# Performance work log

Measured on AMD Instinct MI355X. Metric: run time of the kernel, lower is better.

Reference implementation:

```python
import jax, jax.numpy as jnp
import numpy as np

VOCAB, D, SLOTS, K = 50257, 512, 16, 3
B, T_FULL = 64, 2049
EPS_LN = 1e-5


def setup_inputs() -> dict:
    key = jax.random.key(0)
    ks = jax.random.split(key, 12)
    u = jax.random.uniform(ks[0], (B, T_FULL - 1), jnp.float32)
    gumbel = -jnp.log(-jnp.log(u + 1e-8) + 1e-8)
    s = 0.02
    return {
        "seq": jax.random.randint(ks[1], (B, T_FULL), 0, VOCAB),
        "temperature": jnp.ones((), jnp.float32),
        "gumbel": gumbel,
        "embed": jax.random.normal(ks[2], (VOCAB, D), jnp.float32) * s,
        "W1": jax.random.normal(ks[3], (D, 2 * D), jnp.float32) * s,
        "b1": jnp.zeros((2 * D,), jnp.float32),
        "W2": jax.random.normal(ks[4], (2 * D, D), jnp.float32) * s,
        "b2": jnp.zeros((D,), jnp.float32),
        "gamma": jnp.ones((D,), jnp.float32),
        "beta": jnp.zeros((D,), jnp.float32),
        "Wg": jax.random.normal(ks[5], (D,), jnp.float32) * s,
        "bg": jnp.zeros((), jnp.float32),
        "Wr": jax.random.normal(ks[6], (D, D), jnp.float32) * s,
        "br": jnp.zeros((D,), jnp.float32),
        "Wo": jax.random.normal(ks[7], (D, VOCAB), jnp.float32) * s,
        "bo": jnp.zeros((VOCAB,), jnp.float32),
    }


def reference(seq, temperature, gumbel, embed, W1, b1, W2, b2, gamma, beta, Wg, bg, Wr, br, Wo, bo):
    # Encoder: embed -> FFN residual -> LayerNorm
    h = embed[seq]                                        # [B, T+1, D]
    ff = jnp.maximum(h @ W1 + b1, 0.0) @ W2 + b2
    x = h + ff
    mu = jnp.mean(x, -1, keepdims=True)
    var = jnp.mean((x - mu) ** 2, -1, keepdims=True)
    hiddens = (x - mu) * jax.lax.rsqrt(var + EPS_LN) * gamma + beta

    context = hiddens[:, :-1, :]                          # [B, T, D]
    gate = context @ Wg + bg                              # [B, T]

    # gumbel top-k with straight-through mask (forward value = hard mask)
    perturbed = (gate + gumbel) / temperature
    _, idx = jax.lax.top_k(perturbed, K)                  # [B, K]
    mask = jnp.zeros_like(gate).at[jnp.arange(B)[:, None], idx].set(1.0)
    soft = jax.nn.softmax(perturbed, axis=-1)
    sel = mask + soft - jax.lax.stop_gradient(soft)

    # gather selected hidden states, scatter_add into memory slots
    gw = jnp.take_along_axis(sel, idx, axis=1)            # [B, K]
    gh = jnp.take_along_axis(context, idx[..., None], axis=1)  # [B, K, D]
    weighted = gh * gw[..., None]
    slot_idx = jnp.arange(K) % SLOTS
    mem = jnp.zeros((B, SLOTS, D), hiddens.dtype).at[:, slot_idx, :].add(weighted)

    # attention read with last-position query
    q = hiddens[:, -1, :] @ Wr + br                       # [B, D]
    scores = jnp.einsum('bsd,bd->bs', mem, q)
    attn = jax.nn.softmax(scores, axis=-1)
    ctx = jnp.einsum('bs,bsd->bd', attn, mem)
    return ctx @ Wo + bo                                  # [B, vocab]
```

## Files before the change

kernel.cpp:

```cpp
#include <hip/hip_runtime.h>
#include <math.h>

#define TFULL 2049
#define TCTX  2048
#define Vm    50257

typedef __attribute__((ext_vector_type(8))) short bf16x8;
typedef __attribute__((ext_vector_type(4))) float f32x4;

__device__ __forceinline__ float wred64(float v){
  #pragma unroll
  for (int m = 1; m < 64; m <<= 1) v += __shfl_xor(v, m, 64);
  return v;
}
__device__ __forceinline__ short bf16_rn(float x){
  union { float f; unsigned u; } c; c.f = x;
  unsigned r = c.u + 0x7fff + ((c.u >> 16) & 1);
  return (short)(r >> 16);
}
__device__ __forceinline__ float bf16_f(short s){
  union { float f; unsigned u; } c; c.u = ((unsigned)(unsigned short)s) << 16;
  return c.f;
}

#define FMA4(ACC_, S_, W_)                         \
  (ACC_).x = fmaf((S_), (W_).x, (ACC_).x);         \
  (ACC_).y = fmaf((S_), (W_).y, (ACC_).y);         \
  (ACC_).z = fmaf((S_), (W_).z, (ACC_).z);         \
  (ACC_).w = fmaf((S_), (W_).w, (ACC_).w);

__global__ void k0_setup(const float* __restrict__ gamma, const float* __restrict__ beta,
                         const float* __restrict__ Wg, float* __restrict__ scal){
  const int t = threadIdx.x;
  float wg = Wg[t];
  float g  = gamma[t]*wg, bw = beta[t]*wg;
  scal[2 + t] = g;
  g = wred64(g); bw = wred64(bw);
  __shared__ float ra[8], rb[8];
  if ((t & 63) == 0){ ra[t>>6] = g; rb[t>>6] = bw; }
  __syncthreads();
  if (t == 0){
    float G = 0.f, Bw = 0.f;
    #pragma unroll
    for (int i = 0; i < 8; ++i){ G += ra[i]; Bw += rb[i]; }
    scal[0] = G; scal[1] = Bw;
  }
}

__global__ __launch_bounds__(256) void kpack(const float* __restrict__ W, int N, int KB,
                                             short* __restrict__ hi, short* __restrict__ lo){
  int i = blockIdx.x*256 + threadIdx.x;
  if (i >= KB*N*4) return;
  int kq = i & 3;
  int n  = (i >> 2) % N;
  int kb = i / (N*4);
  const float* src = W + (kb*32 + kq*8)*N + n;
  bf16x8 h8, l8;
  #pragma unroll
  for (int j = 0; j < 8; ++j){
    float w = src[j*N];
    short h = bf16_rn(w);
    h8[j] = h;
    l8[j] = bf16_rn(w - bf16_f(h));
  }
  *(bf16x8*)(hi + i*8) = h8;
  *(bf16x8*)(lo + i*8) = l8;
}

__global__ __launch_bounds__(512, 2) void k1_main(
    const int*   __restrict__ seq,   const float* __restrict__ temp,
    const float* __restrict__ gumbel,const float* __restrict__ embed,
    const short* __restrict__ W1h,   const short* __restrict__ W1l,
    const float* __restrict__ b1,
    const short* __restrict__ W2h,   const short* __restrict__ W2l,
    const float* __restrict__ b2,
    const float* __restrict__ gamma, const float* __restrict__ beta,
    const float* __restrict__ bg,
    const float* __restrict__ scal,
    float* __restrict__ pert, float* __restrict__ qh)
{
  __shared__ short Ah[8*2560];
  __shared__ short Al[8*2560];
  __shared__ short Rbuf[32768];
  __shared__ float Xq[512];
  __shared__ int   srow[64];
  __shared__ float redS1[512], redS2[512], redSG[512];
  __shared__ float redMu[64], redRs[64];

  short* Rh = Rbuf;
  short* Rl = Rbuf + 16384;

  const int t    = threadIdx.x;
  const int tile = blockIdx.x;
  const int lane = t & 63;
  const int wv   = t >> 6;
  const int mrow = lane & 15;
  const int kq   = lane >> 4;
  const int crow0 = kq*4;

  if (t < 64) srow[t] = seq[tile*64 + t];
  __syncthreads();

  const f32x4* __restrict__ embv = (const f32x4*)embed;

  auto stageA = [&](int hh){
    #pragma unroll
    for (int k = 0; k < 8; ++k){
      int idx = k*512 + t;
      int tok = idx >> 6, c4 = idx & 63;
      f32x4 v = __builtin_nontemporal_load(embv + srow[tok]*128 + hh*64 + c4);
      int dl = c4*4;
      int base = (dl>>5)*2560 + tok*40 + ((dl>>3)&3)*8 + (dl&7);
      short h0 = bf16_rn(v[0]), h1 = bf16_rn(v[1]), h2 = bf16_rn(v[2]), h3 = bf16_rn(v[3]);
      Ah[base+0] = h0; Ah[base+1] = h1; Ah[base+2] = h2; Ah[base+3] = h3;
      Al[base+0] = bf16_rn(v[0] - bf16_f(h0));
      Al[base+1] = bf16_rn(v[1] - bf16_f(h1));
      Al[base+2] = bf16_rn(v[2] - bf16_f(h2));
      Al[base+3] = bf16_rn(v[3] - bf16_f(h3));
    }
  };

  f32x4 ff[4][4];
  #pragma unroll
  for (int i = 0; i < 4; ++i)
    #pragma unroll
    for (int j = 0; j < 4; ++j) ff[i][j] = (f32x4){0.f,0.f,0.f,0.f};

  for (int ch = 0; ch < 4; ++ch){
    f32x4 acc[2][4];
    #pragma unroll
    for (int i = 0; i < 2; ++i)
      #pragma unroll
      for (int j = 0; j < 4; ++j) acc[i][j] = (f32x4){0.f,0.f,0.f,0.f};

    auto g1 = [&](int hh){
      #pragma unroll 4
      for (int kbr = 0; kbr < 8; ++kbr){
        bf16x8 ah[4], al[4];
        #pragma unroll
        for (int mt = 0; mt < 4; ++mt){
          ah[mt] = *(const bf16x8*)(Ah + kbr*2560 + (mrow + 16*mt)*40 + kq*8);
          al[mt] = *(const bf16x8*)(Al + kbr*2560 + (mrow + 16*mt)*40 + kq*8);
        }
        int kbg = hh*8 + kbr;
        #pragma unroll
        for (int nt = 0; nt < 2; ++nt){
          int n = ch*256 + wv*32 + nt*16 + mrow;
          int off = ((kbg*1024 + n)*4 + kq)*8;
          bf16x8 bh = *(const bf16x8*)(W1h + off);
          bf16x8 bl = *(const bf16x8*)(W1l + off);
          #pragma unroll
          for (int mt = 0; mt < 4; ++mt){
            acc[nt][mt] = __builtin_amdgcn_mfma_f32_16x16x32_bf16(ah[mt], bh, acc[nt][mt], 0,0,0);
            acc[nt][mt] = __builtin_amdgcn_mfma_f32_16x16x32_bf16(al[mt], bh, acc[nt][mt], 0,0,0);
            acc[nt][mt] = __builtin_amdgcn_mfma_f32_16x16x32_bf16(ah[mt], bl, acc[nt][mt], 0,0,0);
          }
        }
      }
    };

    stageA(0);
    __syncthreads();
    g1(0);
    __syncthreads();
    stageA(1);
    __syncthreads();
    g1(1);
    __syncthreads();

    #pragma unroll
    for (int nt = 0; nt < 2; ++nt){
      int jcol = wv*32 + nt*16 + mrow;
      float bb = b1[ch*256 + jcol];
      int rbase = (jcol>>5)*2048 + ((jcol>>3)&3)*8 + (jcol&7);
      #pragma unroll
      for (int mt = 0; mt < 4; ++mt){
        #pragma unroll
        for (int r = 0; r < 4; ++r){
          int tok = mt*16 + crow0 + r;
          float a = fmaxf(acc[nt][mt][r] + bb, 0.f);
          short h = bf16_rn(a);
          Rh[rbase + tok*32] = h;
          Rl[rbase + tok*32] = bf16_rn(a - bf16_f(h));
        }
      }
    }
    __syncthreads();

    #pragma unroll 2
    for (int kb = 0; kb < 8; ++kb){
      bf16x8 rh[4], rl[4];
      #pragma unroll
      for (int mt = 0; mt < 4; ++mt){
        rh[mt] = *(const bf16x8*)(Rh + kb*2048 + (mrow + 16*mt)*32 + kq*8);
        rl[mt] = *(const bf16x8*)(Rl + kb*2048 + (mrow + 16*mt)*32 + kq*8);
      }
      int kbg = ch*8 + kb;
      #pragma unroll
      for (int nt = 0; nt < 4; ++nt){
        int n = wv*64 + nt*16 + mrow;
        int off = ((kbg*512 + n)*4 + kq)*8;
        bf16x8 bh = *(const bf16x8*)(W2h + off);
        bf16x8 bl = *(const bf16x8*)(W2l + off);
        #pragma unroll
        for (int mt = 0; mt < 4; ++mt){
          ff[nt][mt] = __builtin_amdgcn_mfma_f32_16x16x32_bf16(rh[mt], bh, ff[nt][mt], 0,0,0);
          ff[nt][mt] = __builtin_amdgcn_mfma_f32_16x16x32_bf16(rl[mt], bh, ff[nt][mt], 0,0,0);
          ff[nt][mt] = __builtin_amdgcn_mfma_f32_16x16x32_bf16(rh[mt], bl, ff[nt][mt], 0,0,0);
        }
      }
    }
  }

  __syncthreads();
  float* hbuf = (float*)Rbuf;
  #pragma unroll
  for (int k = 0; k < 8; ++k){
    int idx = k*512 + t;
    int tok = idx >> 6, c4 = idx & 63;
    f32x4 v = __builtin_nontemporal_load(embv + srow[tok]*128 + c4);
    f32x4 hv;
    #pragma unroll
    for (int j = 0; j < 4; ++j){
      short hi = bf16_rn(v[j]);
      hv[j] = bf16_f(hi) + bf16_f(bf16_rn(v[j] - bf16_f(hi)));
    }
    *(f32x4*)(hbuf + tok*256 + c4*4) = hv;
  }
  __syncthreads();

  const float G1 = scal[0], BW = scal[1];
  const float* gWg = scal + 2;
  const float bgv  = bg[0];
  const float invT = 1.0f / temp[0];
  int rem  = (tile*64) % 2049;
  int qtok = 2048 - rem;

  float ps1[4][4], ps2[4][4], psg[4][4];
  #pragma unroll
  for (int mt = 0; mt < 4; ++mt)
    #pragma unroll
    for (int r = 0; r < 4; ++r){ ps1[mt][r]=0.f; ps2[mt][r]=0.f; psg[mt][r]=0.f; }

  #pragma unroll
  for (int nt = 0; nt < 4; ++nt){
    int d = wv*64 + nt*16 + mrow;
    float b2v = b2[d];
    float gw  = gWg[d];
    if (wv >= 4){
      int abase = ((d - 256)>>5)*2560 + ((d>>3)&3)*8 + (d&7);
      #pragma unroll
      for (int mt = 0; mt < 4; ++mt){
        #pragma unroll
        for (int r = 0; r < 4; ++r){
          int tok = mt*16 + crow0 + r;
          float h = bf16_f(Ah[abase + tok*40]) + bf16_f(Al[abase + tok*40]);
          float x = h + ff[nt][mt][r] + b2v;
          ps1[mt][r] += x;
          ps2[mt][r] = fmaf(x, x, ps2[mt][r]);
          psg[mt][r] = fmaf(x, gw, psg[mt][r]);
          if (tok == qtok) Xq[d] = x;
        }
      }
    } else {
      #pragma unroll
      for (int mt = 0; mt < 4; ++mt){
        #pragma unroll
        for (int r = 0; r < 4; ++r){
          int tok = mt*16 + crow0 + r;
          float h = hbuf[tok*256 + d];
          float x = h + ff[nt][mt][r] + b2v;
          ps1[mt][r] += x;
          ps2[mt][r] = fmaf(x, x, ps2[mt][r]);
          psg[mt][r] = fmaf(x, gw, psg[mt][r]);
          if (tok == qtok) Xq[d] = x;
        }
      }
    }
  }
  #pragma unroll
  for (int mt = 0; mt < 4; ++mt){
    #pragma unroll
    for (int r = 0; r < 4; ++r){
      float a = ps1[mt][r], b = ps2[mt][r], c = psg[mt][r];
      #pragma unroll
      for (int m = 1; m < 16; m <<= 1){
        a += __shfl_xor(a, m, 64);
        b += __shfl_xor(b, m, 64);
        c += __shfl_xor(c, m, 64);
      }
      if (mrow == 0){
        int tok = mt*16 + crow0 + r;
        redS1[tok*8 + wv] = a;
        redS2[tok*8 + wv] = b;
        redSG[tok*8 + wv] = c;
      }
    }
  }
  __syncthreads();

  if (t < 64){
    float S1 = 0.f, S2 = 0.f, SG = 0.f;
    #pragma unroll
    for (int w = 0; w < 8; ++w){
      S1 += redS1[t*8 + w];
      S2 += redS2[t*8 + w];
      SG += redSG[t*8 + w];
    }
    float mu  = S1 * (1.f/512.f);
    float var = S2 * (1.f/512.f) - mu*mu;
    float rs  = rsqrtf(var + 1e-5f);
    redMu[t] = mu; redRs[t] = rs;
    int id  = tile*64 + t;
    int b   = id / 2049;
    int pos = id - b*2049;
    if (pos < TCTX){
      float gate = rs*(SG - mu*G1) + BW + bgv;
      float pv = (gate + __builtin_nontemporal_load(gumbel + b*TCTX + pos)) * invT;
      __builtin_nontemporal_store(pv, pert + b*TCTX + pos);
    }
  }
  __syncthreads();

  if (qtok < 64 && t < 256){
    int id = tile*64 + qtok;
    int b  = id / 2049;
    float mu = redMu[qtok], rs = redRs[qtok];
    int d = t*2;
    qh[b*512 + d]     = (Xq[d]  -mu)*rs*gamma[d]   + beta[d];
    qh[b*512 + d + 1] = (Xq[d+1]-mu)*rs*gamma[d+1] + beta[d+1];
  }
}

__global__ __launch_bounds__(256) void k2_topk(const float* __restrict__ pert,
                                               int* __restrict__ idxw){
  __shared__ float v[2048];
  __shared__ float wvv[256];
  __shared__ int   wii[256];
  const int b = blockIdx.x, t = threadIdx.x;
  for (int i = t; i < 2048; i += 256) v[i] = pert[b*TCTX + i];
  __syncthreads();
  for (int r = 0; r < 3; ++r){
    float best = -INFINITY; int bi = 1<<30;
    for (int i = t; i < 2048; i += 256){
      float x = v[i];
      if (x > best || (x == best && i < bi)){ best = x; bi = i; }
    }
    wvv[t] = best; wii[t] = bi;
    __syncthreads();
    for (int s = 128; s > 0; s >>= 1){
      if (t < s){
        float ov = wvv[t+s]; int oi = wii[t+s];
        if (ov > wvv[t] || (ov == wvv[t] && oi < wii[t])){ wvv[t] = ov; wii[t] = oi; }
      }
      __syncthreads();
    }
    if (t == 0){ idxw[b*3 + r] = wii[0]; v[wii[0]] = -INFINITY; }
    __syncthreads();
  }
}

__global__ __launch_bounds__(256) void k3_rows(const int* __restrict__ seq,
    const float* __restrict__ embed, const float* __restrict__ W1, const float* __restrict__ b1,
    const float* __restrict__ W2,    const float* __restrict__ b2,
    const float* __restrict__ gamma, const float* __restrict__ beta,
    const int* __restrict__ idxw, float* __restrict__ memr)
{
  __shared__ float hs[512];
  __shared__ float rbuf[1024];
  __shared__ float red1[4], red2[4];
  const int t   = threadIdx.x;
  const int blk = blockIdx.x;
  const int b = blk / 3, kk = blk - b*3;
  const int pos = idxw[b*3 + kk];
  const int row = seq[b*TFULL + pos];
  ((float2*)hs)[t] = ((const float2*)(embed + row*512))[t];
  __syncthreads();
  const float4* W1v = (const float4*)W1;
  float4 a = make_float4(0,0,0,0);
  #pragma unroll 4
  for (int d = 0; d < 512; ++d){
    float xb = hs[d];
    float4 wq = W1v[d*256 + t];
    FMA4(a, xb, wq);
  }
  float4 bq = ((const float4*)b1)[t];
  float4 r;
  r.x = fmaxf(a.x+bq.x, 0.f); r.y = fmaxf(a.y+bq.y, 0.f);
  r.z = fmaxf(a.z+bq.z, 0.f); r.w = fmaxf(a.w+bq.w, 0.f);
  ((float4*)rbuf)[t] = r;
  __syncthreads();
  const float2* W2v2 = (const float2*)W2;
  float fx = 0.f, fy = 0.f;
  #pragma unroll 4
  for (int j = 0; j < 1024; ++j){
    float rb = rbuf[j];
    float2 wq = W2v2[j*256 + t];
    fx = fmaf(rb, wq.x, fx); fy = fmaf(rb, wq.y, fy);
  }
  float2 b2q = ((const float2*)b2)[t];
  float2 hx  = ((float2*)hs)[t];
  float x0 = hx.x + fx + b2q.x;
  float x1 = hx.y + fy + b2q.y;
  float s1 = wred64(x0 + x1);
  float s2 = wred64(x0*x0 + x1*x1);
  if ((t & 63) == 0){ red1[t>>6] = s1; red2[t>>6] = s2; }
  __syncthreads();
  float S1 = red1[0]+red1[1]+red1[2]+red1[3];
  float S2 = red2[0]+red2[1]+red2[2]+red2[3];
  float mu  = S1*(1.f/512.f);
  float var = S2*(1.f/512.f) - mu*mu;
  float rs  = rsqrtf(var + 1e-5f);
  const int dd = t*2;
  memr[(b*3+kk)*512 + dd]     = (x0-mu)*rs*gamma[dd]   + beta[dd];
  memr[(b*3+kk)*512 + dd + 1] = (x1-mu)*rs*gamma[dd+1] + beta[dd+1];
}

__global__ __launch_bounds__(256) void k4_attn(const float* __restrict__ qh,
    const float* __restrict__ Wr, const float* __restrict__ br,
    const float* __restrict__ memr, float* __restrict__ ctxT)
{
  __shared__ float hq[512];
  __shared__ float red[12];
  const int t = threadIdx.x, b = blockIdx.x;
  ((float2*)hq)[t] = ((const float2*)(qh + b*512))[t];
  __syncthreads();
  const float2* Wrv = (const float2*)Wr;
  float qx = 0.f, qy = 0.f;
  #pragma unroll 4
  for (int d = 0; d < 512; ++d){
    float hb = hq[d];
    float2 wq = Wrv[d*256 + t];
    qx = fmaf(hb, wq.x, qx); qy = fmaf(hb, wq.y, qy);
  }
  float2 brq = ((const float2*)br)[t];
  qx += brq.x; qy += brq.y;
  const int dd = t*2;
  const float* m0 = memr + (b*3+0)*512;
  const float* m1 = memr + (b*3+1)*512;
  const float* m2 = memr + (b*3+2)*512;
  float p0 = wred64(qx*m0[dd] + qy*m0[dd+1]);
  float p1 = wred64(qx*m1[dd] + qy*m1[dd+1]);
  float p2 = wred64(qx*m2[dd] + qy*m2[dd+1]);
  if ((t & 63) == 0){ int w = t>>6; red[w*3+0]=p0; red[w*3+1]=p1; red[w*3+2]=p2; }
  __syncthreads();
  float s0 = red[0]+red[3]+red[6]+red[9];
  float s1 = red[1]+red[4]+red[7]+red[10];
  float s2 = red[2]+red[5]+red[8]+red[11];
  float m  = fmaxf(fmaxf(s0, s1), fmaxf(s2, 0.f));
  float e0 = expf(s0-m), e1 = expf(s1-m), e2 = expf(s2-m);
  float den = e0 + e1 + e2 + 13.f*expf(-m);
  float a0 = e0/den, a1 = e1/den, a2 = e2/den;
  float c0 = a0*m0[dd]   + a1*m1[dd]   + a2*m2[dd];
  float c1 = a0*m0[dd+1] + a1*m1[dd+1] + a2*m2[dd+1];
  ctxT[dd*64 + b]     = c0;
  ctxT[(dd+1)*64 + b] = c1;
}

__global__ __launch_bounds__(256) void k5_out(const float* __restrict__ ctxT,
    const float* __restrict__ Wo, const float* __restrict__ bo,
    float* __restrict__ out)
{
  const int v  = blockIdx.x*256 + threadIdx.x;
  const int vc = v < Vm ? v : Vm-1;
  float acc[64];
  #pragma unroll
  for (int b = 0; b < 64; ++b) acc[b] = 0.f;
  for (int d = 0; d < 512; ++d){
    float w = Wo[d*Vm + vc];
    const float* c = ctxT + d*64;
    #pragma unroll
    for (int b = 0; b < 64; ++b) acc[b] = fmaf(c[b], w, acc[b]);
  }
  if (v < Vm){
    float bb = bo[v];
    #pragma unroll
    for (int b = 0; b < 64; ++b) out[b*Vm + v] = acc[b] + bb;
  }
}

extern "C" void kernel_launch(void* const* d_in, const int* in_sizes, int n_in,
                              void* d_out, int out_size, void* d_ws, size_t ws_size,
                              hipStream_t stream){
  (void)in_sizes; (void)n_in; (void)out_size; (void)ws_size;
  const int*   seq   = (const int*)d_in[0];
  const float* temp  = (const float*)d_in[1];
  const float* gum   = (const float*)d_in[2];
  const float* embed = (const float*)d_in[3];
  const float* W1    = (const float*)d_in[4];
  const float* b1    = (const float*)d_in[5];
  const float* W2    = (const float*)d_in[6];
  const float* b2    = (const float*)d_in[7];
  const float* gamma = (const float*)d_in[8];
  const float* beta  = (const float*)d_in[9];
  const float* Wg    = (const float*)d_in[10];
  const float* bg    = (const float*)d_in[11];
  const float* Wr    = (const float*)d_in[12];
  const float* br    = (const float*)d_in[13];
  const float* Wo    = (const float*)d_in[14];
  const float* bo    = (const float*)d_in[15];
  float* out = (float*)d_out;

  float* wsf  = (float*)d_ws;
  float* pert = wsf;
  float* qh   = wsf + 131072;
  float* memr = wsf + 163840;
  float* ctxT = wsf + 262144;
  float* scal = wsf + 294912;
  int*   idxw = (int*)(wsf + 295936);
  short* W1h  = (short*)(wsf + 296192);
  short* W1l  = W1h + 512*1024;
  short* W2h  = W1l + 512*1024;
  short* W2l  = W2h + 1024*512;

  k0_setup<<<1, 512, 0, stream>>>(gamma, beta, Wg, scal);
  kpack<<<256, 256, 0, stream>>>(W1, 1024, 16, W1h, W1l);
  kpack<<<256, 256, 0, stream>>>(W2, 512, 32, W2h, W2l);
  k1_main<<<2049, 512, 0, stream>>>(seq, temp, gum, embed, W1h, W1l, b1,
                                    W2h, W2l, b2, gamma, beta, bg, scal, pert, qh);
  k2_topk<<<64, 256, 0, stream>>>(pert, idxw);
  k3_rows<<<192, 256, 0, stream>>>(seq, embed, W1, b1, W2, b2, gamma, beta, idxw, memr);
  k4_attn<<<64, 256, 0, stream>>>(qh, Wr, br, memr, ctxT);
  k5_out<<<197, 256, 0, stream>>>(ctxT, Wo, bo, out);
}
```

Before: 2.226 ms.

## Double-buffer MFMA operand loads and repack LDS tiles into k-quad-major layout

Both FFN GEMM inner loops now prefetch the next k-block's A fragments (from LDS) and B fragments (from global) into register double buffers while the current block's MFMAs run, with fully unrolled loops and precomputed offsets. The LDS layout for the embedding and ReLU staging buffers changes from padded row-major (stride 40) to a kq-major packing with stride 8, which shrinks LDS use and allows 4-wide vector stores. Nontemporal embedding loads are replaced by plain loads. The double buffers raise register pressure under launch_bounds(512,2), which risks spills, and the new layout may change LDS bank-conflict behaviour.

```diff
diff --git a/kernel.cpp b/kernel.cpp
--- a/kernel.cpp
+++ b/kernel.cpp
@@ -6,6 +6,7 @@
 #define Vm    50257
 
 typedef __attribute__((ext_vector_type(8))) short bf16x8;
+typedef __attribute__((ext_vector_type(4))) short s16x4;
 typedef __attribute__((ext_vector_type(4))) float f32x4;
 
 __device__ __forceinline__ float wred64(float v){
@@ -79,8 +80,8 @@
     const float* __restrict__ scal,
     float* __restrict__ pert, float* __restrict__ qh)
 {
-  __shared__ short Ah[8*2560];
-  __shared__ short Al[8*2560];
+  __shared__ short Ah[8*2048];
+  __shared__ short Al[8*2048];
   __shared__ short Rbuf[32768];
   __shared__ float Xq[512];
   __shared__ int   srow[64];
@@ -108,15 +109,15 @@
     for (int k = 0; k < 8; ++k){
       int idx = k*512 + t;
       int tok = idx >> 6, c4 = idx & 63;
-      f32x4 v = __builtin_nontemporal_load(embv + srow[tok]*128 + hh*64 + c4);
+      f32x4 v = embv[srow[tok]*128 + hh*64 + c4];
       int dl = c4*4;
-      int base = (dl>>5)*2560 + tok*40 + ((dl>>3)&3)*8 + (dl&7);
+      int base = (dl>>5)*2048 + ((dl>>3)&3)*512 + tok*8 + (dl&7);
       short h0 = bf16_rn(v[0]), h1 = bf16_rn(v[1]), h2 = bf16_rn(v[2]), h3 = bf16_rn(v[3]);
-      Ah[base+0] = h0; Ah[base+1] = h1; Ah[base+2] = h2; Ah[base+3] = h3;
-      Al[base+0] = bf16_rn(v[0] - bf16_f(h0));
-      Al[base+1] = bf16_rn(v[1] - bf16_f(h1));
-      Al[base+2] = bf16_rn(v[2] - bf16_f(h2));
-      Al[base+3] = bf16_rn(v[3] - bf16_f(h3));
+      *(s16x4*)(Ah + base) = (s16x4){h0, h1, h2, h3};
+      *(s16x4*)(Al + base) = (s16x4){ bf16_rn(v[0] - bf16_f(h0)),
+                                      bf16_rn(v[1] - bf16_f(h1)),
+                                      bf16_rn(v[2] - bf16_f(h2)),
+                                      bf16_rn(v[3] - bf16_f(h3)) };
     }
   };
 
@@ -126,6 +127,13 @@
     #pragma unroll
     for (int j = 0; j < 4; ++j) ff[i][j] = (f32x4){0.f,0.f,0.f,0.f};
 
+  const int aoff = kq*512 + mrow*8;
+  int boff2[4];
+  #pragma unroll
+  for (int nt = 0; nt < 4; ++nt)
+    boff2[nt] = (wv*64 + nt*16 + mrow)*32 + kq*8;
+
+  #pragma unroll 1
   for (int ch = 0; ch < 4; ++ch){
     f32x4 acc[2][4];
     #pragma unroll
@@ -133,29 +141,48 @@
       #pragma unroll
       for (int j = 0; j < 4; ++j) acc[i][j] = (f32x4){0.f,0.f,0.f,0.f};
 
+    int boff1[2];
+    #pragma unroll
+    for (int nt = 0; nt < 2; ++nt)
+      boff1[nt] = (ch*256 + wv*32 + nt*16 + mrow)*32 + kq*8;
+
     auto g1 = [&](int hh){
-      #pragma unroll 4
+      const short* whB = W1h + hh*262144;
+      const short* wlB = W1l + hh*262144;
+      bf16x8 ah[2][4], al[2][4], bh[2][2], bl[2][2];
+      #pragma unroll
+      for (int mt = 0; mt < 4; ++mt){
+        ah[0][mt] = *(const bf16x8*)(Ah + aoff + mt*128);
+        al[0][mt] = *(const bf16x8*)(Al + aoff + mt*128);
+      }
+      #pragma unroll
+      for (int nt = 0; nt < 2; ++nt){
+        bh[0][nt] = *(const bf16x8*)(whB + boff1[nt]);
+        bl[0][nt] = *(const bf16x8*)(wlB + boff1[nt]);
+      }
+      #pragma unroll
       for (int kbr = 0; kbr < 8; ++kbr){
-        bf16x8 ah[4], al[4];
-        #pragma unroll
-        for (int mt = 0; mt < 4; ++mt){
-          ah[mt] = *(const bf16x8*)(Ah + kbr*2560 + (mrow + 16*mt)*40 + kq*8);
-          al[mt] = *(const bf16x8*)(Al + kbr*2560 + (mrow + 16*mt)*40 + kq*8);
-        }
-        int kbg = hh*8 + kbr;
-        #pragma unroll
-        for (int nt = 0; nt < 2; ++nt){
-          int n = ch*256 + wv*32 + nt*16 + mrow;
-          int off = ((kbg*1024 + n)*4 + kq)*8;
-          bf16x8 bh = *(const bf16x8*)(W1h + off);
-          bf16x8 bl = *(const bf16x8*)(W1l + off);
+        const int cur = kbr & 1, nxt = cur ^ 1;
+        if (kbr < 7){
           #pragma unroll
           for (int mt = 0; mt < 4; ++mt){
-            acc[nt][mt] = __builtin_amdgcn_mfma_f32_16x16x32_bf16(ah[mt], bh, acc[nt][mt], 0,0,0);
-            acc[nt][mt] = __builtin_amdgcn_mfma_f32_16x16x32_bf16(al[mt], bh, acc[nt][mt], 0,0,0);
-            acc[nt][mt] = __builtin_amdgcn_mfma_f32_16x16x32_bf16(ah[mt], bl, acc[nt][mt], 0,0,0);
+            ah[nxt][mt] = *(const bf16x8*)(Ah + (kbr+1)*2048 + aoff + mt*128);
+            al[nxt][mt] = *(const bf16x8*)(Al + (kbr+1)*2048 + aoff + mt*128);
+          }
+          #pragma unroll
+          for (int nt = 0; nt < 2; ++nt){
+            bh[nxt][nt] = *(const bf16x8*)(whB + (kbr+1)*32768 + boff1[nt]);
+            bl[nxt][nt] = *(const bf16x8*)(wlB + (kbr+1)*32768 + boff1[nt]);
           }
         }
+        #pragma unroll
+        for (int nt = 0; nt < 2; ++nt)
+          #pragma unroll
+          for (int mt = 0; mt < 4; ++mt){
+            acc[nt][mt] = __builtin_amdgcn_mfma_f32_16x16x32_bf16(ah[cur][mt], bh[cur][nt], acc[nt][mt], 0,0,0);
+            acc[nt][mt] = __builtin_amdgcn_mfma_f32_16x16x32_bf16(al[cur][mt], bh[cur][nt], acc[nt][mt], 0,0,0);
+            acc[nt][mt] = __builtin_amdgcn_mfma_f32_16x16x32_bf16(ah[cur][mt], bl[cur][nt], acc[nt][mt], 0,0,0);
+          }
       }
     };
 
@@ -172,7 +199,7 @@
     for (int nt = 0; nt < 2; ++nt){
       int jcol = wv*32 + nt*16 + mrow;
       float bb = b1[ch*256 + jcol];
-      int rbase = (jcol>>5)*2048 + ((jcol>>3)&3)*8 + (jcol&7);
+      int rbase = (jcol>>5)*2048 + ((jcol>>3)&3)*512 + (jcol&7);
       #pragma unroll
       for (int mt = 0; mt < 4; ++mt){
         #pragma unroll
@@ -180,34 +207,50 @@
           int tok = mt*16 + crow0 + r;
           float a = fmaxf(acc[nt][mt][r] + bb, 0.f);
           short h = bf16_rn(a);
-          Rh[rbase + tok*32] = h;
-          Rl[rbase + tok*32] = bf16_rn(a - bf16_f(h));
+          Rh[rbase + tok*8] = h;
+          Rl[rbase + tok*8] = bf16_rn(a - bf16_f(h));
         }
       }
     }
     __syncthreads();
 
-    #pragma unroll 2
-    for (int kb = 0; kb < 8; ++kb){
-      bf16x8 rh[4], rl[4];
+    {
+      const short* w2hB = W2h + ch*131072;
+      const short* w2lB = W2l + ch*131072;
+      bf16x8 rh2[2][4], rl2[2][4], bh2[2][4], bl2[2][4];
       #pragma unroll
       for (int mt = 0; mt < 4; ++mt){
-        rh[mt] = *(const bf16x8*)(Rh + kb*2048 + (mrow + 16*mt)*32 + kq*8);
-        rl[mt] = *(const bf16x8*)(Rl + kb*2048 + (mrow + 16*mt)*32 + kq*8);
-      }
-      int kbg = ch*8 + kb;
+        rh2[0][mt] = *(const bf16x8*)(Rh + aoff + mt*128);
+        rl2[0][mt] = *(const bf16x8*)(Rl + aoff + mt*128);
+      }
       #pragma unroll
       for (int nt = 0; nt < 4; ++nt){
-        int n = wv*64 + nt*16 + mrow;
-        int off = ((kbg*512 + n)*4 + kq)*8;
-        bf16x8 bh = *(const bf16x8*)(W2h + off);
-        bf16x8 bl = *(const bf16x8*)(W2l + off);
+        bh2[0][nt] = *(const bf16x8*)(w2hB + boff2[nt]);
+        bl2[0][nt] = *(const bf16x8*)(w2lB + boff2[nt]);
+      }
+      #pragma unroll
+      for (int kb = 0; kb < 8; ++kb){
+        const int cur = kb & 1, nxt = cur ^ 1;
+        if (kb < 7){
+          #pragma unroll
+          for (int mt = 0; mt < 4; ++mt){
+            rh2[nxt][mt] = *(const bf16x8*)(Rh + (kb+1)*2048 + aoff + mt*128);
+            rl2[nxt][mt] = *(const bf16x8*)(Rl + (kb+1)*2048 + aoff + mt*128);
+          }
+          #pragma unroll
+          for (int nt = 0; nt < 4; ++nt){
+            bh2[nxt][nt] = *(const bf16x8*)(w2hB + (kb+1)*16384 + boff2[nt]);
+            bl2[nxt][nt] = *(const bf16x8*)(w2lB + (kb+1)*16384 + boff2[nt]);
+          }
+        }
         #pragma unroll
-        for (int mt = 0; mt < 4; ++mt){
-          ff[nt][mt] = __builtin_amdgcn_mfma_f32_16x16x32_bf16(rh[mt], bh, ff[nt][mt], 0,0,0);
-          ff[nt][mt] = __builtin_amdgcn_mfma_f32_16x16x32_bf16(rl[mt], bh, ff[nt][mt], 0,0,0);
-          ff[nt][mt] = __builtin_amdgcn_mfma_f32_16x16x32_bf16(rh[mt], bl, ff[nt][mt], 0,0,0);
-        }
+        for (int nt = 0; nt < 4; ++nt)
+          #pragma unroll
+          for (int mt = 0; mt < 4; ++mt){
+            ff[nt][mt] = __builtin_amdgcn_mfma_f32_16x16x32_bf16(rh2[cur][mt], bh2[cur][nt], ff[nt][mt], 0,0,0);
+            ff[nt][mt] = __builtin_amdgcn_mfma_f32_16x16x32_bf16(rl2[cur][mt], bh2[cur][nt], ff[nt][mt], 0,0,0);
+            ff[nt][mt] = __builtin_amdgcn_mfma_f32_16x16x32_bf16(rh2[cur][mt], bl2[cur][nt], ff[nt][mt], 0,0,0);
+          }
       }
     }
   }
@@ -218,7 +261,7 @@
   for (int k = 0; k < 8; ++k){
     int idx = k*512 + t;
     int tok = idx >> 6, c4 = idx & 63;
-    f32x4 v = __builtin_nontemporal_load(embv + srow[tok]*128 + c4);
+    f32x4 v = embv[srow[tok]*128 + c4];
     f32x4 hv;
     #pragma unroll
     for (int j = 0; j < 4; ++j){
@@ -248,13 +291,13 @@
     float b2v = b2[d];
     float gw  = gWg[d];
     if (wv >= 4){
-      int abase = ((d - 256)>>5)*2560 + ((d>>3)&3)*8 + (d&7);
+      int abase = ((d - 256)>>5)*2048 + ((d>>3)&3)*512 + (d&7);
       #pragma unroll
       for (int mt = 0; mt < 4; ++mt){
         #pragma unroll
         for (int r = 0; r < 4; ++r){
           int tok = mt*16 + crow0 + r;
-          float h = bf16_f(Ah[abase + tok*40]) + bf16_f(Al[abase + tok*40]);
+          float h = bf16_f(Ah[abase + tok*8]) + bf16_f(Al[abase + tok*8]);
           float x = h + ff[nt][mt][r] + b2v;
           ps1[mt][r] += x;
           ps2[mt][r] = fmaf(x, x, ps2[mt][r]);
```

New measurement: 2.145 ms. 3.7% less time.
